# Kernel tuning notes

Measured on AMD Instinct MI355X. Metric: run time of the kernel, lower is better.

Reference implementation:

```python
import jax, jax.numpy as jnp
import numpy as np

N_NODES = 50000
N_EDGES = 800000
IN_DIM, HID_DIM, OUT_DIM = 128, 96, 40


def setup_inputs() -> dict:
    key = jax.random.key(0)
    ks = jax.random.split(key, 8)
    x = jax.random.normal(ks[0], (N_NODES, IN_DIM), dtype=jnp.float32)
    edge_src = jax.random.randint(ks[1], (N_EDGES,), 0, N_NODES, dtype=jnp.int32)
    edge_dst = jax.random.randint(ks[2], (N_EDGES,), 0, N_NODES, dtype=jnp.int32)
    edge_val = jax.random.uniform(ks[3], (N_EDGES,), dtype=jnp.float32)
    W1 = jax.random.normal(ks[4], (IN_DIM, HID_DIM), dtype=jnp.float32) * 0.05
    b1 = jax.random.normal(ks[5], (HID_DIM,), dtype=jnp.float32) * 0.05
    W2 = jax.random.normal(ks[6], (HID_DIM, OUT_DIM), dtype=jnp.float32) * 0.05
    b2 = jax.random.normal(ks[7], (OUT_DIM,), dtype=jnp.float32) * 0.05
    return {"x": x, "edge_val": edge_val, "W1": W1, "b1": b1,
            "W2": W2, "b2": b2, "edge_src": edge_src, "edge_dst": edge_dst}


def _spmm(edge_src, edge_dst, edge_val, dense, num_nodes):
    # out[i] = sum_{e: dst[e]==i} val[e] * dense[src[e]]  (COO sparse @ dense)
    msgs = edge_val[:, None] * dense[edge_src]  # [E, D]
    return jax.ops.segment_sum(msgs, edge_dst, num_segments=num_nodes)


def reference(x, edge_val, W1, b1, W2, b2, edge_src, edge_dst):
    n = x.shape[0]
    # GraphConv 1: support = x @ W1; out = A @ support + b1
    h = _spmm(edge_src, edge_dst, edge_val, x @ W1, n) + b1
    h = jax.nn.relu(h)  # dropout is identity in eval mode
    # GraphConv 2
    out = _spmm(edge_src, edge_dst, edge_val, h @ W2, n) + b2
    return jax.nn.log_softmax(out, axis=1)
```

## Files before the change

kernel.cpp:

```cpp
#include <hip/hip_runtime.h>
#include <hip/hip_fp16.h>
#include <math.h>

#define N_NODES 50000
#define N_EDGES 800000
#define IN_DIM 128
#define HID_DIM 96
#define OUT_DIM 40
#define CAP 48
#define NB_G1 782
#define NB_FILL 3125

typedef __attribute__((ext_vector_type(8))) unsigned short ushort8_t;
typedef __attribute__((ext_vector_type(8))) short short8_t;
typedef __attribute__((ext_vector_type(4))) float floatx4_t;

static __device__ __forceinline__ unsigned short f2bf(float f) {
    unsigned int u = __float_as_uint(f);
    u += 0x7FFFu + ((u >> 16) & 1u);
    return (unsigned short)(u >> 16);
}
static __device__ __forceinline__ float bf2f(unsigned short h) {
    return __uint_as_float(((unsigned int)h) << 16);
}

__global__ __launch_bounds__(256) void gemm1_fill_kernel(
    const float* __restrict__ x, const float* __restrict__ W1,
    unsigned short* __restrict__ supb,
    const int* __restrict__ esrc, const int* __restrict__ edst,
    const float* __restrict__ eval, int* __restrict__ cnt,
    unsigned int* __restrict__ recs, int n) {
    const int b = blockIdx.x;
    const int t = threadIdx.x;

    if (b >= NB_G1) {
        int e = (b - NB_G1) * 256 + t;
        if (e < N_EDGES) {
            int d = edst[e];
            int pos = atomicAdd(&cnt[d], 1);
            if (pos < CAP) {
                unsigned int rec = (unsigned int)esrc[e] |
                    ((unsigned int)__half_as_ushort(__float2half(eval[e])) << 16);
                recs[(size_t)d * CAP + pos] = rec;
            }
        }
        return;
    }

    __shared__ unsigned short sB[24 * 64 * 8];
    for (int i = t; i < IN_DIM * HID_DIM; i += 256) {
        int k = i / HID_DIM, nn = i - k * HID_DIM;
        int c = k >> 5, q = (k >> 3) & 3, j = k & 7;
        int g = nn >> 4, l16 = nn & 15;
        sB[(((c * 6 + g) * 64) + q * 16 + l16) * 8 + j] = f2bf(W1[i]);
    }
    __syncthreads();

    const int wave = t >> 6, lane = t & 63;
    const int m = lane & 15, q = lane >> 4;
    const int r0 = b * 64 + wave * 16;
    const int row = r0 + m;
    const bool rok = row < n;

    floatx4_t acc[6];
    #pragma unroll
    for (int g = 0; g < 6; ++g) acc[g] = (floatx4_t){0.f, 0.f, 0.f, 0.f};

    #pragma unroll
    for (int c = 0; c < 4; ++c) {
        float4 a0 = make_float4(0.f, 0.f, 0.f, 0.f), a1 = a0;
        if (rok) {
            const float4* xp = (const float4*)(x + (size_t)row * IN_DIM + c * 32 + q * 8);
            a0 = xp[0];
            a1 = xp[1];
        }
        short8_t af;
        af[0] = (short)f2bf(a0.x); af[1] = (short)f2bf(a0.y);
        af[2] = (short)f2bf(a0.z); af[3] = (short)f2bf(a0.w);
        af[4] = (short)f2bf(a1.x); af[5] = (short)f2bf(a1.y);
        af[6] = (short)f2bf(a1.z); af[7] = (short)f2bf(a1.w);
        #pragma unroll
        for (int g = 0; g < 6; ++g) {
            short8_t bf = *(const short8_t*)&sB[(((c * 6 + g) * 64) + lane) * 8];
            acc[g] = __builtin_amdgcn_mfma_f32_16x16x32_bf16(af, bf, acc[g], 0, 0, 0);
        }
    }

    #pragma unroll
    for (int r = 0; r < 4; ++r) {
        int ro = r0 + q * 4 + r;
        if (ro < n) {
            #pragma unroll
            for (int g = 0; g < 6; ++g)
                supb[(size_t)ro * HID_DIM + g * 16 + m] = f2bf(acc[g][r]);
        }
    }
}

__global__ __launch_bounds__(256) void gather1_gemm2_kernel(
    const unsigned short* __restrict__ supb, const unsigned int* __restrict__ recs,
    const int* __restrict__ cnt, const float* __restrict__ b1,
    const float* __restrict__ W2, unsigned short* __restrict__ yb) {
    __shared__ float sH[21][HID_DIM + 4];
    __shared__ float sW2[HID_DIM * OUT_DIM];
    __shared__ unsigned int sRec[21][52];
    const int t = threadIdx.x;
    const int dst0 = blockIdx.x * 21;
    const int g = t / 12, l = t % 12;
    const int dst = dst0 + g;
    const bool active = (t < 252) && (dst < N_NODES);

    for (int i = t; i < HID_DIM * OUT_DIM / 4; i += 256)
        ((float4*)sW2)[i] = ((const float4*)W2)[i];

    for (int i = t; i < 21 * 12; i += 256) {
        int gg = i / 12, qq = i % 12;
        int dd = dst0 + gg;
        if (dd < N_NODES)
            ((uint4*)&sRec[gg][0])[qq] = ((const uint4*)(recs + (size_t)dd * CAP))[qq];
    }
    __syncthreads();

    if (active) {
        int deg = cnt[dst];
        deg = deg < CAP ? deg : CAP;
        float acc[8] = {};
        const int c8 = l;
        for (int p = 0; p < deg; ++p) {
            unsigned int r = sRec[g][p];
            int s = (int)(r & 0xFFFFu);
            float v = __half2float(__ushort_as_half((unsigned short)(r >> 16)));
            ushort8_t sv = ((const ushort8_t*)(supb + (size_t)s * HID_DIM))[c8];
            #pragma unroll
            for (int j = 0; j < 8; ++j) acc[j] += v * bf2f(sv[j]);
        }
        float4 r0, r1;
        r0.x = fmaxf(acc[0] + b1[c8 * 8 + 0], 0.f);
        r0.y = fmaxf(acc[1] + b1[c8 * 8 + 1], 0.f);
        r0.z = fmaxf(acc[2] + b1[c8 * 8 + 2], 0.f);
        r0.w = fmaxf(acc[3] + b1[c8 * 8 + 3], 0.f);
        r1.x = fmaxf(acc[4] + b1[c8 * 8 + 4], 0.f);
        r1.y = fmaxf(acc[5] + b1[c8 * 8 + 5], 0.f);
        r1.z = fmaxf(acc[6] + b1[c8 * 8 + 6], 0.f);
        r1.w = fmaxf(acc[7] + b1[c8 * 8 + 7], 0.f);
        float4* hp = (float4*)&sH[g][c8 * 8];
        hp[0] = r0;
        hp[1] = r1;
    }
    __syncthreads();

    for (int idx = t; idx < 21 * OUT_DIM; idx += 256) {
        int d = idx / OUT_DIM, c = idx % OUT_DIM;
        int dd = dst0 + d;
        if (dd >= N_NODES) continue;
        const float4* hr = (const float4*)&sH[d][0];
        float s = 0.f;
        #pragma unroll
        for (int k4 = 0; k4 < HID_DIM / 4; ++k4) {
            float4 hv = hr[k4];
            s += hv.x * sW2[(k4 * 4 + 0) * OUT_DIM + c]
               + hv.y * sW2[(k4 * 4 + 1) * OUT_DIM + c]
               + hv.z * sW2[(k4 * 4 + 2) * OUT_DIM + c]
               + hv.w * sW2[(k4 * 4 + 3) * OUT_DIM + c];
        }
        yb[(size_t)dd * OUT_DIM + c] = f2bf(s);
    }
}

__global__ __launch_bounds__(256) void gather2_lsm_kernel(
    const unsigned short* __restrict__ yb, const unsigned int* __restrict__ recs,
    const int* __restrict__ cnt, const float* __restrict__ b2,
    float* __restrict__ out) {
    __shared__ unsigned int sRec[50][52];
    __shared__ float part[256];
    __shared__ float smax[50];
    __shared__ float ssum[50];
    const int t = threadIdx.x;
    const int g = t / 5;
    const int c8 = t % 5;
    int dst = blockIdx.x * 50 + g;
    bool active = (t < 250) && (dst < N_NODES);

    for (int i = t; i < 50 * 12; i += 256) {
        int gg = i / 12, qq = i % 12;
        int dd = blockIdx.x * 50 + gg;
        if (dd < N_NODES)
            ((uint4*)&sRec[gg][0])[qq] = ((const uint4*)(recs + (size_t)dd * CAP))[qq];
    }
    __syncthreads();

    float acc[8] = {};
    if (active) {
        int deg = cnt[dst];
        deg = deg < CAP ? deg : CAP;
        for (int p = 0; p < deg; ++p) {
            unsigned int r = sRec[g][p];
            int s = (int)(r & 0xFFFFu);
            float v = __half2float(__ushort_as_half((unsigned short)(r >> 16)));
            ushort8_t sv = ((const ushort8_t*)(yb + (size_t)s * OUT_DIM))[c8];
            #pragma unroll
            for (int j = 0; j < 8; ++j) acc[j] += v * bf2f(sv[j]);
        }
        #pragma unroll
        for (int j = 0; j < 8; ++j) acc[j] += b2[c8 * 8 + j];
    }
    float lmax = -INFINITY;
    #pragma unroll
    for (int j = 0; j < 8; ++j) lmax = fmaxf(lmax, acc[j]);
    part[t] = active ? lmax : -INFINITY;
    __syncthreads();
    if (t < 50) {
        float m = part[t * 5];
        #pragma unroll
        for (int i = 1; i < 5; ++i) m = fmaxf(m, part[t * 5 + i]);
        smax[t] = m;
    }
    __syncthreads();
    float m = active ? smax[g] : 0.f;
    float lsum = 0.f;
    #pragma unroll
    for (int j = 0; j < 8; ++j) lsum += expf(acc[j] - m);
    part[t] = active ? lsum : 0.f;
    __syncthreads();
    if (t < 50) {
        float s = 0.f;
        #pragma unroll
        for (int i = 0; i < 5; ++i) s += part[t * 5 + i];
        ssum[t] = logf(s);
    }
    __syncthreads();
    if (active) {
        float ls = ssum[g];
        float* op = out + (size_t)dst * OUT_DIM + c8 * 8;
        ((float4*)op)[0] = make_float4(acc[0] - m - ls, acc[1] - m - ls,
                                       acc[2] - m - ls, acc[3] - m - ls);
        ((float4*)op)[1] = make_float4(acc[4] - m - ls, acc[5] - m - ls,
                                       acc[6] - m - ls, acc[7] - m - ls);
    }
}

extern "C" void kernel_launch(void* const* d_in, const int* in_sizes, int n_in,
                              void* d_out, int out_size, void* d_ws, size_t ws_size,
                              hipStream_t stream) {
    const float* x        = (const float*)d_in[0];
    const float* edge_val = (const float*)d_in[1];
    const float* W1       = (const float*)d_in[2];
    const float* b1       = (const float*)d_in[3];
    const float* W2       = (const float*)d_in[4];
    const float* b2       = (const float*)d_in[5];
    const int*   esrc     = (const int*)d_in[6];
    const int*   edst     = (const int*)d_in[7];
    float* out = (float*)d_out;

    int*   cnt  = (int*)d_ws;
    unsigned int* recs = (unsigned int*)(cnt + 50048);
    unsigned short* supb = (unsigned short*)(recs + (size_t)N_NODES * CAP);
    unsigned short* yb   = supb + (size_t)N_NODES * HID_DIM;

    hipMemsetAsync(cnt, 0, N_NODES * sizeof(int), stream);
    gemm1_fill_kernel<<<NB_G1 + NB_FILL, 256, 0, stream>>>(
        x, W1, supb, esrc, edst, edge_val, cnt, recs, N_NODES);
    gather1_gemm2_kernel<<<(N_NODES + 20) / 21, 256, 0, stream>>>(
        supb, recs, cnt, b1, W2, yb);
    gather2_lsm_kernel<<<(N_NODES + 49) / 50, 256, 0, stream>>>(
        yb, recs, cnt, b2, out);
}
```

Baseline: 187.1 us.

## Split each destination's edge gather across two thread groups with shared-memory reduction

Both gather kernels now give each destination node twice as many threads: the edge list is split into even and odd halves, and the partial sums are combined through shared memory before the bias, ReLU/GEMM2 or log-softmax steps. Blocks now cover fewer destinations, so twice as many blocks are launched. The aim is more memory-level parallelism per node and shorter serial gather loops, which should hide latency on the random row gathers. In exchange it adds an extra barrier and shared-memory round trip, and the W2 tile is reloaded into shared memory by twice as many blocks in the first kernel.

```diff
diff --git a/kernel.cpp b/kernel.cpp
--- a/kernel.cpp
+++ b/kernel.cpp
@@ -10,6 +10,8 @@
 #define CAP 48
 #define NB_G1 782
 #define NB_FILL 3125
+#define NDST3 10
+#define NDST4 25
 
 typedef __attribute__((ext_vector_type(8))) unsigned short ushort8_t;
 typedef __attribute__((ext_vector_type(8))) short short8_t;
@@ -101,19 +103,20 @@
     const unsigned short* __restrict__ supb, const unsigned int* __restrict__ recs,
     const int* __restrict__ cnt, const float* __restrict__ b1,
     const float* __restrict__ W2, unsigned short* __restrict__ yb) {
-    __shared__ float sH[21][HID_DIM + 4];
+    __shared__ float sH[NDST3][HID_DIM + 4];
     __shared__ float sW2[HID_DIM * OUT_DIM];
-    __shared__ unsigned int sRec[21][52];
+    __shared__ unsigned int sRec[NDST3][52];
+    __shared__ float sPart[NDST3][12][8];
     const int t = threadIdx.x;
-    const int dst0 = blockIdx.x * 21;
-    const int g = t / 12, l = t % 12;
+    const int dst0 = blockIdx.x * NDST3;
+    const int g = t / 24, l = t % 24;
+    const int c8 = l % 12, half = l / 12;
     const int dst = dst0 + g;
-    const bool active = (t < 252) && (dst < N_NODES);
+    const bool active = (t < NDST3 * 24) && (dst < N_NODES);
 
     for (int i = t; i < HID_DIM * OUT_DIM / 4; i += 256)
         ((float4*)sW2)[i] = ((const float4*)W2)[i];
-
-    for (int i = t; i < 21 * 12; i += 256) {
+    for (int i = t; i < NDST3 * 12; i += 256) {
         int gg = i / 12, qq = i % 12;
         int dd = dst0 + gg;
         if (dd < N_NODES)
@@ -121,12 +124,11 @@
     }
     __syncthreads();
 
+    float acc[8] = {};
     if (active) {
         int deg = cnt[dst];
         deg = deg < CAP ? deg : CAP;
-        float acc[8] = {};
-        const int c8 = l;
-        for (int p = 0; p < deg; ++p) {
+        for (int p = half; p < deg; p += 2) {
             unsigned int r = sRec[g][p];
             int s = (int)(r & 0xFFFFu);
             float v = __half2float(__ushort_as_half((unsigned short)(r >> 16)));
@@ -134,22 +136,32 @@
             #pragma unroll
             for (int j = 0; j < 8; ++j) acc[j] += v * bf2f(sv[j]);
         }
+        if (half == 1) {
+            float4* pp = (float4*)&sPart[g][c8][0];
+            pp[0] = make_float4(acc[0], acc[1], acc[2], acc[3]);
+            pp[1] = make_float4(acc[4], acc[5], acc[6], acc[7]);
+        }
+    }
+    __syncthreads();
+    if (active && half == 0) {
+        const float4* pp = (const float4*)&sPart[g][c8][0];
+        float4 p0 = pp[0], p1 = pp[1];
         float4 r0, r1;
-        r0.x = fmaxf(acc[0] + b1[c8 * 8 + 0], 0.f);
-        r0.y = fmaxf(acc[1] + b1[c8 * 8 + 1], 0.f);
-        r0.z = fmaxf(acc[2] + b1[c8 * 8 + 2], 0.f);
-        r0.w = fmaxf(acc[3] + b1[c8 * 8 + 3], 0.f);
-        r1.x = fmaxf(acc[4] + b1[c8 * 8 + 4], 0.f);
-        r1.y = fmaxf(acc[5] + b1[c8 * 8 + 5], 0.f);
-        r1.z = fmaxf(acc[6] + b1[c8 * 8 + 6], 0.f);
-        r1.w = fmaxf(acc[7] + b1[c8 * 8 + 7], 0.f);
+        r0.x = fmaxf(acc[0] + p0.x + b1[c8 * 8 + 0], 0.f);
+        r0.y = fmaxf(acc[1] + p0.y + b1[c8 * 8 + 1], 0.f);
+        r0.z = fmaxf(acc[2] + p0.z + b1[c8 * 8 + 2], 0.f);
+        r0.w = fmaxf(acc[3] + p0.w + b1[c8 * 8 + 3], 0.f);
+        r1.x = fmaxf(acc[4] + p1.x + b1[c8 * 8 + 4], 0.f);
+        r1.y = fmaxf(acc[5] + p1.y + b1[c8 * 8 + 5], 0.f);
+        r1.z = fmaxf(acc[6] + p1.z + b1[c8 * 8 + 6], 0.f);
+        r1.w = fmaxf(acc[7] + p1.w + b1[c8 * 8 + 7], 0.f);
         float4* hp = (float4*)&sH[g][c8 * 8];
         hp[0] = r0;
         hp[1] = r1;
     }
     __syncthreads();
 
-    for (int idx = t; idx < 21 * OUT_DIM; idx += 256) {
+    for (int idx = t; idx < NDST3 * OUT_DIM; idx += 256) {
         int d = idx / OUT_DIM, c = idx % OUT_DIM;
         int dd = dst0 + d;
         if (dd >= N_NODES) continue;
@@ -171,19 +183,21 @@
     const unsigned short* __restrict__ yb, const unsigned int* __restrict__ recs,
     const int* __restrict__ cnt, const float* __restrict__ b2,
     float* __restrict__ out) {
-    __shared__ unsigned int sRec[50][52];
-    __shared__ float part[256];
-    __shared__ float smax[50];
-    __shared__ float ssum[50];
+    __shared__ unsigned int sRec[NDST4][52];
+    __shared__ float sPart[NDST4][5][8];
+    __shared__ float part[NDST4 * 5];
+    __shared__ float smax[NDST4];
+    __shared__ float ssum[NDST4];
     const int t = threadIdx.x;
-    const int g = t / 5;
-    const int c8 = t % 5;
-    int dst = blockIdx.x * 50 + g;
-    bool active = (t < 250) && (dst < N_NODES);
-
-    for (int i = t; i < 50 * 12; i += 256) {
+    const int dst0 = blockIdx.x * NDST4;
+    const int g = t / 10, l = t % 10;
+    const int c8 = l % 5, half = l / 5;
+    const int dst = dst0 + g;
+    const bool active = (t < NDST4 * 10) && (dst < N_NODES);
+
+    for (int i = t; i < NDST4 * 12; i += 256) {
         int gg = i / 12, qq = i % 12;
-        int dd = blockIdx.x * 50 + gg;
+        int dd = dst0 + gg;
         if (dd < N_NODES)
             ((uint4*)&sRec[gg][0])[qq] = ((const uint4*)(recs + (size_t)dd * CAP))[qq];
     }
@@ -193,7 +207,7 @@
     if (active) {
         int deg = cnt[dst];
         deg = deg < CAP ? deg : CAP;
-        for (int p = 0; p < deg; ++p) {
+        for (int p = half; p < deg; p += 2) {
             unsigned int r = sRec[g][p];
             int s = (int)(r & 0xFFFFu);
             float v = __half2float(__ushort_as_half((unsigned short)(r >> 16)));
@@ -201,35 +215,51 @@
             #pragma unroll
             for (int j = 0; j < 8; ++j) acc[j] += v * bf2f(sv[j]);
         }
+        if (half == 1) {
+            float4* pp = (float4*)&sPart[g][c8][0];
+            pp[0] = make_float4(acc[0], acc[1], acc[2], acc[3]);
+            pp[1] = make_float4(acc[4], acc[5], acc[6], acc[7]);
+        }
+    }
+    __syncthreads();
+
+    const bool own = active && (half == 0);
+    if (own) {
+        const float4* pp = (const float4*)&sPart[g][c8][0];
+        float4 p0 = pp[0], p1 = pp[1];
+        acc[0] += p0.x; acc[1] += p0.y; acc[2] += p0.z; acc[3] += p0.w;
+        acc[4] += p1.x; acc[5] += p1.y; acc[6] += p1.z; acc[7] += p1.w;
         #pragma unroll
         for (int j = 0; j < 8; ++j) acc[j] += b2[c8 * 8 + j];
-    }
-    float lmax = -INFINITY;
-    #pragma unroll
-    for (int j = 0; j < 8; ++j) lmax = fmaxf(lmax, acc[j]);
-    part[t] = active ? lmax : -INFINITY;
-    __syncthreads();
-    if (t < 50) {
+        float lmax = -INFINITY;
+        #pragma unroll
+        for (int j = 0; j < 8; ++j) lmax = fmaxf(lmax, acc[j]);
+        part[g * 5 + c8] = lmax;
+    }
+    __syncthreads();
+    if (t < NDST4 && (dst0 + t) < N_NODES) {
         float m = part[t * 5];
         #pragma unroll
         for (int i = 1; i < 5; ++i) m = fmaxf(m, part[t * 5 + i]);
         smax[t] = m;
     }
     __syncthreads();
-    float m = active ? smax[g] : 0.f;
-    float lsum = 0.f;
-    #pragma unroll
-    for (int j = 0; j < 8; ++j) lsum += expf(acc[j] - m);
-    part[t] = active ? lsum : 0.f;
-    __syncthreads();
-    if (t < 50) {
+    float m = own ? smax[g] : 0.f;
+    if (own) {
+        float lsum = 0.f;
+        #pragma unroll
+        for (int j = 0; j < 8; ++j) lsum += expf(acc[j] - m);
+        part[g * 5 + c8] = lsum;
+    }
+    __syncthreads();
+    if (t < NDST4 && (dst0 + t) < N_NODES) {
         float s = 0.f;
         #pragma unroll
         for (int i = 0; i < 5; ++i) s += part[t * 5 + i];
         ssum[t] = logf(s);
     }
     __syncthreads();
-    if (active) {
+    if (own) {
         float ls = ssum[g];
         float* op = out + (size_t)dst * OUT_DIM + c8 * 8;
         ((float4*)op)[0] = make_float4(acc[0] - m - ls, acc[1] - m - ls,
@@ -260,8 +290,8 @@
     hipMemsetAsync(cnt, 0, N_NODES * sizeof(int), stream);
     gemm1_fill_kernel<<<NB_G1 + NB_FILL, 256, 0, stream>>>(
         x, W1, supb, esrc, edst, edge_val, cnt, recs, N_NODES);
-    gather1_gemm2_kernel<<<(N_NODES + 20) / 21, 256, 0, stream>>>(
+    gather1_gemm2_kernel<<<(N_NODES + NDST3 - 1) / NDST3, 256, 0, stream>>>(
         supb, recs, cnt, b1, W2, yb);
-    gather2_lsm_kernel<<<(N_NODES + 49) / 50, 256, 0, stream>>>(
+    gather2_lsm_kernel<<<(N_NODES + NDST4 - 1) / NDST4, 256, 0, stream>>>(
         yb, recs, cnt, b2, out);
 }
```

Measured after the change: 193.7 us. +3.5%, slower.
